# Performance work log

Hardware: AMD Instinct MI355X
Metric: run time of the kernel (lower is better)

The kernel has to match this reference:

```python
import jax, jax.numpy as jnp
import numpy as np

MARGIN = 0.3


def setup_inputs() -> dict:
    key = jax.random.key(0)
    k1, k2 = jax.random.split(key)
    B, D, N_IDS = 8192, 256, 512
    emb = jax.random.normal(k1, (B, D), dtype=jnp.float32)
    emb = emb / jnp.linalg.norm(emb, axis=1, keepdims=True)  # L2-normalized as docstring states
    labels = jax.random.randint(k2, (B,), 0, N_IDS, dtype=jnp.int64)
    return {"embeddings": emb, "labels": labels}


def reference(embeddings, labels):
    B = embeddings.shape[0]
    # pairwise Euclidean distance via cosine similarity (embeddings are L2-normalized)
    sim = jnp.matmul(embeddings, embeddings.T)              # (B, B)
    dist = jnp.sqrt(jnp.clip(2.0 - 2.0 * sim, 0.0) + 1e-12)
    same = labels[:, None] == labels[None, :]               # (B, B)
    eye = jnp.eye(B, dtype=bool)
    pos_mask = same & ~eye
    neg_mask = ~same
    neg_inf = jnp.asarray(-jnp.inf, dist.dtype)
    pos_inf = jnp.asarray(jnp.inf, dist.dtype)
    dist_ap = jnp.max(jnp.where(pos_mask, dist, neg_inf), axis=1)  # hardest positive per anchor
    dist_an = jnp.min(jnp.where(neg_mask, dist, pos_inf), axis=1)  # hardest negative per anchor
    valid = jnp.any(pos_mask, axis=1) & jnp.any(neg_mask, axis=1)
    # MarginRankingLoss(dist_an, dist_ap, y=1) = mean(relu(dist_ap - dist_an + margin)) over valid anchors
    per = jnp.maximum(dist_ap - dist_an + MARGIN, 0.0)
    per = jnp.where(valid, per, 0.0)
    n_valid = jnp.sum(valid.astype(dist.dtype))
    loss = jnp.where(n_valid > 0, jnp.sum(per) / jnp.maximum(n_valid, 1.0), 0.0)
    return loss
```

## Files before the change

### kernel.cpp

```cpp
#include <hip/hip_runtime.h>
#include <hip/hip_bf16.h>


#define BDIM 8192
#define DDIM 256

typedef short bf16x8 __attribute__((ext_vector_type(8)));
typedef float f32x4  __attribute__((ext_vector_type(4)));
typedef unsigned short u16;

static __device__ __forceinline__ bf16x8 ld_frag(const u16* p) {
    return *reinterpret_cast<const bf16x8*>(p);
}

static __device__ __forceinline__ u16 f2bf(float f) {
    union { float f; unsigned int u; } x; x.f = f;
    unsigned int u = x.u;
    unsigned int r = u + 0x7fffu + ((u >> 16) & 1u);
    return (u16)(r >> 16);
}

static __device__ __forceinline__ void gload_lds16(const u16* g, u16* l) {
    __builtin_amdgcn_global_load_lds(
        (const __attribute__((address_space(1))) unsigned int*)g,
        (__attribute__((address_space(3))) unsigned int*)l, 16, 0, 0);
}

__global__ __launch_bounds__(256) void cvt_init_kernel(const float* __restrict__ in,
                                                       u16* __restrict__ out,
                                                       int* __restrict__ minpos,
                                                       int* __restrict__ maxneg) {
    int i = blockIdx.x * 256 + threadIdx.x;
    const float4 v = reinterpret_cast<const float4*>(in)[i];
    ushort4 o;
    o.x = f2bf(v.x); o.y = f2bf(v.y); o.z = f2bf(v.z); o.w = f2bf(v.w);
    reinterpret_cast<ushort4*>(out)[i] = o;
    if (i < BDIM) {
        minpos[i] = 0x7f800000;
        maxneg[i] = 0;
    }
}

__global__ __launch_bounds__(256, 2) void triplet_main(const u16* __restrict__ Ebf,
                                                       const int* __restrict__ labels,
                                                       int* __restrict__ minpos,
                                                       int* __restrict__ maxneg) {
    __shared__ __align__(16) u16 smem[2][64 * DDIM];

    const int tid  = threadIdx.x;
    const int w    = tid >> 6;
    const int l    = tid & 63;
    const int quad = l >> 4;
    const int r16  = l & 15;

    const int mblk  = blockIdx.x * 128 + w * 32;
    const int nbase = blockIdx.y * 1024;

    bf16x8 a[2][8];
#pragma unroll
    for (int ms = 0; ms < 2; ++ms) {
        const u16* ap = Ebf + (size_t)(mblk + ms * 16 + r16) * DDIM + quad * 8;
#pragma unroll
        for (int k = 0; k < 8; ++k) a[ms][k] = ld_frag(ap + k * 32);
    }

    int lab_row[2][4];
#pragma unroll
    for (int ms = 0; ms < 2; ++ms)
#pragma unroll
        for (int r = 0; r < 4; ++r)
            lab_row[ms][r] = labels[mblk + ms * 16 + quad * 4 + r];

    float minp[2][4], maxn[2][4];
#pragma unroll
    for (int ms = 0; ms < 2; ++ms)
#pragma unroll
        for (int r = 0; r < 4; ++r) { minp[ms][r] = __builtin_inff(); maxn[ms][r] = 0.0f; }

    const int qs  = quad ^ (r16 & 3);
    const int s4  = (r16 >> 2) & 1;

    {
        const int n0 = nbase;
#pragma unroll
        for (int it = 0; it < 8; ++it) {
            const int q = it * 256 + tid;
            const int r = q >> 5;
            const int c = (q & 31) ^ (r & 7);
            gload_lds16(Ebf + ((size_t)(n0 + r) << 8) + c * 8,
                        &smem[0][0] + it * 2048 + w * 512);
        }
    }

    for (int nn = 0; nn < 16; ++nn) {
        const int cur = nn & 1;
        const int n0  = nbase + nn * 64;

        __syncthreads();

        if (nn + 1 < 16) {
            const int n1 = n0 + 64;
#pragma unroll
            for (int it = 0; it < 8; ++it) {
                const int q = it * 256 + tid;
                const int r = q >> 5;
                const int c = (q & 31) ^ (r & 7);
                gload_lds16(Ebf + ((size_t)(n1 + r) << 8) + c * 8,
                            &smem[cur ^ 1][0] + it * 2048 + w * 512);
            }
        }

        f32x4 acc[2][4];
#pragma unroll
        for (int ms = 0; ms < 2; ++ms)
#pragma unroll
            for (int nt = 0; nt < 4; ++nt)
                acc[ms][nt] = (f32x4){0.f, 0.f, 0.f, 0.f};

        const u16* bb = &smem[cur][0];
        const u16* bnt[4];
#pragma unroll
        for (int nt = 0; nt < 4; ++nt)
            bnt[nt] = bb + (nt * 16 + r16) * DDIM + qs * 8;

#pragma unroll
        for (int k = 0; k < 8; ++k) {
            const int koff = ((k ^ s4) << 5);
            bf16x8 b[4];
#pragma unroll
            for (int nt = 0; nt < 4; ++nt) b[nt] = ld_frag(bnt[nt] + koff);
#pragma unroll
            for (int ms = 0; ms < 2; ++ms)
#pragma unroll
                for (int nt = 0; nt < 4; ++nt)
                    acc[ms][nt] = __builtin_amdgcn_mfma_f32_16x16x32_bf16(
                        a[ms][k], b[nt], acc[ms][nt], 0, 0, 0);
        }

        int lab_c[4];
#pragma unroll
        for (int nt = 0; nt < 4; ++nt) lab_c[nt] = labels[n0 + nt * 16 + r16];
#pragma unroll
        for (int nt = 0; nt < 4; ++nt) {
            const int colg = n0 + nt * 16 + r16;
#pragma unroll
            for (int ms = 0; ms < 2; ++ms) {
#pragma unroll
                for (int r = 0; r < 4; ++r) {
                    const int rowg = mblk + ms * 16 + quad * 4 + r;
                    const float sp2 = acc[ms][nt][r] + 2.0f;
                    if (colg != rowg) {
                        if (lab_c[nt] == lab_row[ms][r]) minp[ms][r] = fminf(minp[ms][r], sp2);
                        else                             maxn[ms][r] = fmaxf(maxn[ms][r], sp2);
                    }
                }
            }
        }
    }

#pragma unroll
    for (int mask = 1; mask <= 8; mask <<= 1) {
#pragma unroll
        for (int ms = 0; ms < 2; ++ms)
#pragma unroll
            for (int r = 0; r < 4; ++r) {
                minp[ms][r] = fminf(minp[ms][r], __shfl_xor(minp[ms][r], mask, 64));
                maxn[ms][r] = fmaxf(maxn[ms][r], __shfl_xor(maxn[ms][r], mask, 64));
            }
    }
    if (r16 == 0) {
#pragma unroll
        for (int ms = 0; ms < 2; ++ms)
#pragma unroll
            for (int r = 0; r < 4; ++r) {
                const int rowg = mblk + ms * 16 + quad * 4 + r;
                atomicMin(minpos + rowg, __float_as_int(minp[ms][r]));
                atomicMax(maxneg + rowg, __float_as_int(maxn[ms][r]));
            }
    }
}

__global__ __launch_bounds__(256) void finalize_kernel(const int* __restrict__ minpos,
                                                       const int* __restrict__ maxneg,
                                                       float* __restrict__ out) {
    __shared__ float ssum[4], scnt[4];
    float sum = 0.f, cnt = 0.f;
    for (int i = threadIdx.x; i < BDIM; i += 256) {
        const float mp = __int_as_float(minpos[i]);
        const float mn = __int_as_float(maxneg[i]);
        if (mp < 1e30f && mn > 0.5f) {
            const float s_ap = mp - 2.0f;
            const float s_an = mn - 2.0f;
            const float dap = sqrtf(fmaxf(2.0f - 2.0f * s_ap, 0.0f) + 1e-12f);
            const float dan = sqrtf(fmaxf(2.0f - 2.0f * s_an, 0.0f) + 1e-12f);
            sum += fmaxf(dap - dan + 0.3f, 0.0f);
            cnt += 1.0f;
        }
    }
#pragma unroll
    for (int off = 32; off > 0; off >>= 1) {
        sum += __shfl_down(sum, off, 64);
        cnt += __shfl_down(cnt, off, 64);
    }
    const int wid = threadIdx.x >> 6;
    if ((threadIdx.x & 63) == 0) { ssum[wid] = sum; scnt[wid] = cnt; }
    __syncthreads();
    if (threadIdx.x == 0) {
        const float S = ssum[0] + ssum[1] + ssum[2] + ssum[3];
        const float C = scnt[0] + scnt[1] + scnt[2] + scnt[3];
        out[0] = (C > 0.f) ? (S / C) : 0.f;
    }
}

extern "C" void kernel_launch(void* const* d_in, const int* in_sizes, int n_in,
                              void* d_out, int out_size, void* d_ws, size_t ws_size,
                              hipStream_t stream) {
    const float* emb    = (const float*)d_in[0];
    const int*   labels = (const int*)d_in[1];
    float*       out    = (float*)d_out;

    u16* Ebf    = (u16*)d_ws;
    int* minpos = (int*)((char*)d_ws + (size_t)BDIM * DDIM * 2);
    int* maxneg = minpos + BDIM;

    cvt_init_kernel<<<dim3((BDIM * DDIM / 4) / 256), dim3(256), 0, stream>>>(emb, Ebf, minpos, maxneg);
    triplet_main<<<dim3(BDIM / 128, BDIM / 1024), dim3(256), 0, stream>>>(Ebf, labels, minpos, maxneg);
    finalize_kernel<<<dim3(1), dim3(256), 0, stream>>>(minpos, maxneg, out);
}
```

Measured before the change: 117.8 us.

## Retile triplet kernel to 64 rows per wave and skip diagonal checks off-diagonal

Each wave now owns 64 anchor rows (4 MFMA row tiles) against 32-column LDS tiles, so every B fragment read from LDS feeds twice as many MFMAs and the shared-memory footprint is halved. The epilogue becomes branch-free select-plus-min/max, with the diagonal exclusion confined to the rare tiles that overlap it, and the +2 bias is moved to the atomics. The finalize kernel uses 1024 threads with an unrolled loop. The cost is more register pressure from the held A fragments and accumulators, which may reduce occupancy under launch_bounds(256,2), and the grid changes shape to 32x16 blocks.

```diff
diff --git a/kernel.cpp b/kernel.cpp
--- a/kernel.cpp
+++ b/kernel.cpp
@@ -45,7 +45,7 @@
                                                        const int* __restrict__ labels,
                                                        int* __restrict__ minpos,
                                                        int* __restrict__ maxneg) {
-    __shared__ __align__(16) u16 smem[2][64 * DDIM];
+    __shared__ __align__(16) u16 smem[2][32 * DDIM];
 
     const int tid  = threadIdx.x;
     const int w    = tid >> 6;
@@ -53,55 +53,52 @@
     const int quad = l >> 4;
     const int r16  = l & 15;
 
-    const int mblk  = blockIdx.x * 128 + w * 32;
-    const int nbase = blockIdx.y * 1024;
-
-    bf16x8 a[2][8];
-#pragma unroll
-    for (int ms = 0; ms < 2; ++ms) {
+    const int mblk  = blockIdx.x * 256 + w * 64;
+    const int nbase = blockIdx.y * 512;
+
+    bf16x8 a[4][8];
+#pragma unroll
+    for (int ms = 0; ms < 4; ++ms) {
         const u16* ap = Ebf + (size_t)(mblk + ms * 16 + r16) * DDIM + quad * 8;
 #pragma unroll
         for (int k = 0; k < 8; ++k) a[ms][k] = ld_frag(ap + k * 32);
     }
 
-    int lab_row[2][4];
-#pragma unroll
-    for (int ms = 0; ms < 2; ++ms)
+    int lab_row[4][4];
+#pragma unroll
+    for (int ms = 0; ms < 4; ++ms)
 #pragma unroll
         for (int r = 0; r < 4; ++r)
             lab_row[ms][r] = labels[mblk + ms * 16 + quad * 4 + r];
 
-    float minp[2][4], maxn[2][4];
-#pragma unroll
-    for (int ms = 0; ms < 2; ++ms)
-#pragma unroll
-        for (int r = 0; r < 4; ++r) { minp[ms][r] = __builtin_inff(); maxn[ms][r] = 0.0f; }
-
-    const int qs  = quad ^ (r16 & 3);
-    const int s4  = (r16 >> 2) & 1;
-
-    {
-        const int n0 = nbase;
-#pragma unroll
-        for (int it = 0; it < 8; ++it) {
-            const int q = it * 256 + tid;
-            const int r = q >> 5;
-            const int c = (q & 31) ^ (r & 7);
-            gload_lds16(Ebf + ((size_t)(n0 + r) << 8) + c * 8,
-                        &smem[0][0] + it * 2048 + w * 512);
-        }
+    float minp[4][4], maxn[4][4];
+#pragma unroll
+    for (int ms = 0; ms < 4; ++ms)
+#pragma unroll
+        for (int r = 0; r < 4; ++r) { minp[ms][r] = __builtin_inff(); maxn[ms][r] = -__builtin_inff(); }
+
+    const int qs = quad ^ (r16 & 3);
+    const int s4 = (r16 >> 2) & 1;
+
+#pragma unroll
+    for (int it = 0; it < 4; ++it) {
+        const int q = it * 256 + tid;
+        const int r = q >> 5;
+        const int c = (q & 31) ^ (r & 7);
+        gload_lds16(Ebf + ((size_t)(nbase + r) << 8) + c * 8,
+                    &smem[0][0] + it * 2048 + w * 512);
     }
 
     for (int nn = 0; nn < 16; ++nn) {
         const int cur = nn & 1;
-        const int n0  = nbase + nn * 64;
+        const int n0  = nbase + nn * 32;
 
         __syncthreads();
 
         if (nn + 1 < 16) {
-            const int n1 = n0 + 64;
-#pragma unroll
-            for (int it = 0; it < 8; ++it) {
+            const int n1 = n0 + 32;
+#pragma unroll
+            for (int it = 0; it < 4; ++it) {
                 const int q = it * 256 + tid;
                 const int r = q >> 5;
                 const int c = (q & 31) ^ (r & 7);
@@ -110,58 +107,73 @@
             }
         }
 
-        f32x4 acc[2][4];
-#pragma unroll
-        for (int ms = 0; ms < 2; ++ms)
-#pragma unroll
-            for (int nt = 0; nt < 4; ++nt)
+        f32x4 acc[4][2];
+#pragma unroll
+        for (int ms = 0; ms < 4; ++ms)
+#pragma unroll
+            for (int nt = 0; nt < 2; ++nt)
                 acc[ms][nt] = (f32x4){0.f, 0.f, 0.f, 0.f};
 
         const u16* bb = &smem[cur][0];
-        const u16* bnt[4];
-#pragma unroll
-        for (int nt = 0; nt < 4; ++nt)
+        const u16* bnt[2];
+#pragma unroll
+        for (int nt = 0; nt < 2; ++nt)
             bnt[nt] = bb + (nt * 16 + r16) * DDIM + qs * 8;
 
 #pragma unroll
         for (int k = 0; k < 8; ++k) {
             const int koff = ((k ^ s4) << 5);
-            bf16x8 b[4];
-#pragma unroll
-            for (int nt = 0; nt < 4; ++nt) b[nt] = ld_frag(bnt[nt] + koff);
-#pragma unroll
-            for (int ms = 0; ms < 2; ++ms)
-#pragma unroll
-                for (int nt = 0; nt < 4; ++nt)
+            bf16x8 b[2];
+#pragma unroll
+            for (int nt = 0; nt < 2; ++nt) b[nt] = ld_frag(bnt[nt] + koff);
+#pragma unroll
+            for (int ms = 0; ms < 4; ++ms)
+#pragma unroll
+                for (int nt = 0; nt < 2; ++nt)
                     acc[ms][nt] = __builtin_amdgcn_mfma_f32_16x16x32_bf16(
                         a[ms][k], b[nt], acc[ms][nt], 0, 0, 0);
         }
 
-        int lab_c[4];
-#pragma unroll
-        for (int nt = 0; nt < 4; ++nt) lab_c[nt] = labels[n0 + nt * 16 + r16];
-#pragma unroll
-        for (int nt = 0; nt < 4; ++nt) {
-            const int colg = n0 + nt * 16 + r16;
-#pragma unroll
-            for (int ms = 0; ms < 2; ++ms) {
-#pragma unroll
-                for (int r = 0; r < 4; ++r) {
-                    const int rowg = mblk + ms * 16 + quad * 4 + r;
-                    const float sp2 = acc[ms][nt][r] + 2.0f;
-                    if (colg != rowg) {
-                        if (lab_c[nt] == lab_row[ms][r]) minp[ms][r] = fminf(minp[ms][r], sp2);
-                        else                             maxn[ms][r] = fmaxf(maxn[ms][r], sp2);
+        int lab_c[2];
+#pragma unroll
+        for (int nt = 0; nt < 2; ++nt) lab_c[nt] = labels[n0 + nt * 16 + r16];
+
+        const bool diagTile = (n0 < mblk + 64) && (mblk < n0 + 32);
+        if (__builtin_expect(diagTile, 0)) {
+#pragma unroll
+            for (int nt = 0; nt < 2; ++nt) {
+                const int colg = n0 + nt * 16 + r16;
+#pragma unroll
+                for (int ms = 0; ms < 4; ++ms)
+#pragma unroll
+                    for (int r = 0; r < 4; ++r) {
+                        const int rowg = mblk + ms * 16 + quad * 4 + r;
+                        const float s = acc[ms][nt][r];
+                        const bool same = (lab_c[nt] == lab_row[ms][r]);
+                        const bool pos  = same && (colg != rowg);
+                        minp[ms][r] = fminf(minp[ms][r], pos  ?  s : __builtin_inff());
+                        maxn[ms][r] = fmaxf(maxn[ms][r], same ? -__builtin_inff() : s);
                     }
-                }
-            }
+            }
+        } else {
+#pragma unroll
+            for (int nt = 0; nt < 2; ++nt)
+#pragma unroll
+                for (int ms = 0; ms < 4; ++ms)
+#pragma unroll
+                    for (int r = 0; r < 4; ++r) {
+                        const float s = acc[ms][nt][r];
+                        const bool same = (lab_c[nt] == lab_row[ms][r]);
+                        minp[ms][r] = fminf(minp[ms][r], same ?  s : __builtin_inff());
+                        maxn[ms][r] = fmaxf(maxn[ms][r], same ? -__builtin_inff() : s);
+                    }
         }
     }
 
 #pragma unroll
     for (int mask = 1; mask <= 8; mask <<= 1) {
 #pragma unroll
-        for (int ms = 0; ms < 2; ++ms)
+        for (int ms = 0; ms < 4; ++ms)
 #pragma unroll
             for (int r = 0; r < 4; ++r) {
                 minp[ms][r] = fminf(minp[ms][r], __shfl_xor(minp[ms][r], mask, 64));
@@ -170,29 +182,29 @@
     }
     if (r16 == 0) {
 #pragma unroll
-        for (int ms = 0; ms < 2; ++ms)
+        for (int ms = 0; ms < 4; ++ms)
 #pragma unroll
             for (int r = 0; r < 4; ++r) {
                 const int rowg = mblk + ms * 16 + quad * 4 + r;
-                atomicMin(minpos + rowg, __float_as_int(minp[ms][r]));
-                atomicMax(maxneg + rowg, __float_as_int(maxn[ms][r]));
-            }
-    }
-}
-
-__global__ __launch_bounds__(256) void finalize_kernel(const int* __restrict__ minpos,
-                                                       const int* __restrict__ maxneg,
-                                                       float* __restrict__ out) {
-    __shared__ float ssum[4], scnt[4];
+                atomicMin(minpos + rowg, __float_as_int(minp[ms][r] + 2.0f));
+                atomicMax(maxneg + rowg, __float_as_int(maxn[ms][r] + 2.0f));
+            }
+    }
+}
+
+__global__ __launch_bounds__(1024) void finalize_kernel(const int* __restrict__ minpos,
+                                                        const int* __restrict__ maxneg,
+                                                        float* __restrict__ out) {
+    __shared__ float ssum[16], scnt[16];
     float sum = 0.f, cnt = 0.f;
-    for (int i = threadIdx.x; i < BDIM; i += 256) {
+#pragma unroll
+    for (int it = 0; it < 8; ++it) {
+        const int i = it * 1024 + threadIdx.x;
         const float mp = __int_as_float(minpos[i]);
         const float mn = __int_as_float(maxneg[i]);
         if (mp < 1e30f && mn > 0.5f) {
-            const float s_ap = mp - 2.0f;
-            const float s_an = mn - 2.0f;
-            const float dap = sqrtf(fmaxf(2.0f - 2.0f * s_ap, 0.0f) + 1e-12f);
-            const float dan = sqrtf(fmaxf(2.0f - 2.0f * s_an, 0.0f) + 1e-12f);
+            const float dap = sqrtf(fmaxf(6.0f - 2.0f * mp, 0.0f) + 1e-12f);
+            const float dan = sqrtf(fmaxf(6.0f - 2.0f * mn, 0.0f) + 1e-12f);
             sum += fmaxf(dap - dan + 0.3f, 0.0f);
             cnt += 1.0f;
         }
@@ -206,8 +218,9 @@
     if ((threadIdx.x & 63) == 0) { ssum[wid] = sum; scnt[wid] = cnt; }
     __syncthreads();
     if (threadIdx.x == 0) {
-        const float S = ssum[0] + ssum[1] + ssum[2] + ssum[3];
-        const float C = scnt[0] + scnt[1] + scnt[2] + scnt[3];
+        float S = 0.f, C = 0.f;
+#pragma unroll
+        for (int i = 0; i < 16; ++i) { S += ssum[i]; C += scnt[i]; }
         out[0] = (C > 0.f) ? (S / C) : 0.f;
     }
 }
@@ -224,6 +237,6 @@
     int* maxneg = minpos + BDIM;
 
     cvt_init_kernel<<<dim3((BDIM * DDIM / 4) / 256), dim3(256), 0, stream>>>(emb, Ebf, minpos, maxneg);
-    triplet_main<<<dim3(BDIM / 128, BDIM / 1024), dim3(256), 0, stream>>>(Ebf, labels, minpos, maxneg);
-    finalize_kernel<<<dim3(1), dim3(256), 0, stream>>>(minpos, maxneg, out);
-}
+    triplet_main<<<dim3(BDIM / 256, BDIM / 512), dim3(256), 0, stream>>>(Ebf, labels, minpos, maxneg);
+    finalize_kernel<<<dim3(1), dim3(1024), 0, stream>>>(minpos, maxneg, out);
+}
```

Result: faster. 105.2 us (-10.7%).
